# Optimization experiments

Measured on AMD Instinct MI355X. Metric: run time of the kernel, lower is better.

The kernel has to match this reference:

```python
import jax, jax.numpy as jnp
import numpy as np

T, B, C, H, W = 9, 8, 256, 56, 56


def setup_inputs() -> dict:
    key = jax.random.key(0)
    k1, k2, k3, k4 = jax.random.split(key, 4)
    feature_maps_sequence = jax.random.normal(k1, (T, B, C, H, W), dtype=jnp.float32)
    # Conv2d(2C, 1, kernel_size=1): weight [1, 2C, 1, 1], bias [1]
    w = jax.random.normal(k2, (1, 2 * C, 1, 1), dtype=jnp.float32) * 0.02
    b = jax.random.normal(k3, (1,), dtype=jnp.float32) * 0.02
    gamma = jax.random.normal(k4, (1,), dtype=jnp.float32)
    return {"feature_maps_sequence": feature_maps_sequence, "w": w, "b": b, "gamma": gamma}


def reference(feature_maps_sequence, w, b, gamma):
    seq = feature_maps_sequence  # [T, B, C, H, W]
    t = seq.shape[0]
    center = seq[t // 2]  # [B, C, H, W]
    c = seq.shape[2]
    # 1x1 conv over concat([center, frame]) == dot with split weight halves + bias
    w_center = w[0, :c, 0, 0]  # [C]
    w_other = w[0, c:, 0, 0]   # [C]
    score_center = jnp.einsum('bchw,c->bhw', center, w_center)          # [B, H, W]
    score_other = jnp.einsum('tbchw,c->tbhw', seq, w_other)             # [T, B, H, W]
    scores = score_center[None] + score_other + b[0]                    # [T, B, H, W]
    attn = jax.nn.softmax(scores, axis=0)                               # softmax over T
    attended = jnp.einsum('tbhw,tbchw->bchw', attn, seq)                # [B, C, H, W]
    return center + gamma * attended
```

## Files before the change

kernel.cpp:

```cpp
#include <hip/hip_runtime.h>
#include <math.h>

#define TT 9
#define BN 8
#define CC 256
#define HW 3136
#define BHW (BN * HW)
#define PIX 64
#define CHUNKS (HW / PIX)
#define CENTER_T 4

__global__ __launch_bounds__(256) void scores_kernel(
    const float* __restrict__ seq, const float* __restrict__ w,
    float* __restrict__ scores) {
  int blk = blockIdx.x;
  int chunk = blk % CHUNKS;
  int tb = blk / CHUNKS;
  int tid = threadIdx.x;
  int pix = tid & 63;
  int cpart = tid >> 6;

  __shared__ float w_other[CC];
  __shared__ float red[256];
  w_other[tid] = w[CC + tid];
  __syncthreads();

  const float* base = seq + (size_t)tb * CC * HW + chunk * PIX + pix;
  int c0 = cpart * 64;
  float acc = 0.f;
#pragma unroll 8
  for (int cl = 0; cl < 64; ++cl) {
    int c = c0 + cl;
    acc = fmaf(base[(size_t)c * HW], w_other[c], acc);
  }
  red[tid] = acc;
  __syncthreads();
  if (cpart == 0) {
    float s = red[pix] + red[64 + pix] + red[128 + pix] + red[192 + pix];
    scores[(size_t)tb * HW + chunk * PIX + pix] = s;
  }
}

__global__ __launch_bounds__(256) void softmax_kernel(float* __restrict__ scores) {
  int p = blockIdx.x * 256 + threadIdx.x;
  float v[TT];
  float m = -1e30f;
#pragma unroll
  for (int t = 0; t < TT; ++t) {
    v[t] = scores[(size_t)t * BHW + p];
    m = fmaxf(m, v[t]);
  }
  float s = 0.f;
#pragma unroll
  for (int t = 0; t < TT; ++t) {
    v[t] = __expf(v[t] - m);
    s += v[t];
  }
  float inv = 1.f / s;
#pragma unroll
  for (int t = 0; t < TT; ++t) scores[(size_t)t * BHW + p] = v[t] * inv;
}

__global__ __launch_bounds__(256) void attend_kernel(
    const float* __restrict__ seq, const float* __restrict__ attn,
    const float* __restrict__ gamma, float* __restrict__ out) {
  int blk = blockIdx.x;
  int chunk = blk % CHUNKS;
  int rest = blk / CHUNKS;
  int cg = rest % (CC / 16);
  int b = rest / (CC / 16);
  int tid = threadIdx.x;
  int pix = tid & 63;
  int csub = tid >> 6;
  int c0 = cg * 16 + csub * 4;
  int hwp = chunk * PIX + pix;

  float a[TT];
#pragma unroll
  for (int t = 0; t < TT; ++t) a[t] = attn[(size_t)t * BHW + b * HW + hwp];

  float acc[4] = {0.f, 0.f, 0.f, 0.f};
  float cen[4];
#pragma unroll
  for (int t = 0; t < TT; ++t) {
    float at = a[t];
#pragma unroll
    for (int i = 0; i < 4; ++i) {
      float v = seq[(((size_t)t * BN + b) * CC + (c0 + i)) * HW + hwp];
      acc[i] = fmaf(at, v, acc[i]);
      if (t == CENTER_T) cen[i] = v;
    }
  }
  float g = gamma[0];
#pragma unroll
  for (int i = 0; i < 4; ++i)
    out[((size_t)b * CC + (c0 + i)) * HW + hwp] = fmaf(g, acc[i], cen[i]);
}

extern "C" void kernel_launch(void* const* d_in, const int* in_sizes, int n_in,
                              void* d_out, int out_size, void* d_ws, size_t ws_size,
                              hipStream_t stream) {
  const float* seq = (const float*)d_in[0];
  const float* w = (const float*)d_in[1];
  const float* gamma = (const float*)d_in[3];
  float* out = (float*)d_out;
  float* scores = (float*)d_ws;

  scores_kernel<<<TT * BN * CHUNKS, 256, 0, stream>>>(seq, w, scores);
  softmax_kernel<<<BHW / 256, 256, 0, stream>>>(scores);
  attend_kernel<<<BN * (CC / 16) * CHUNKS, 256, 0, stream>>>(seq, scores, gamma, out);
}
```

Measured before the change: 358.4 us.

## Fuse score, softmax and attention into a single per-pixel-chunk kernel

Replaces the three-kernel pipeline (scores, softmax, attend) with one kernel. Each block owns 32 pixels of one batch across all channels and all frames: it computes the frame scores with a shared-memory reduction, applies the softmax in place, then re-reads the same sequence slice to form the weighted sum. This removes the scores round trip through global workspace and two extra launches. The second read of the block's slice may be served from cache because it follows soon after the first. In exchange, each block does 16 channel partitions times 9 frames of strided loads, and coalescing drops to 32-pixel (128-byte) rows.

Result: slower. 541.2 us (+51.0%).

```diff
diff --git a/kernel.cpp b/kernel.cpp
--- a/kernel.cpp
+++ b/kernel.cpp
@@ -5,96 +5,91 @@
 #define BN 8
 #define CC 256
 #define HW 3136
-#define BHW (BN * HW)
-#define PIX 64
+#define PIX 32
 #define CHUNKS (HW / PIX)
+#define CPART 16
+#define CPC (CC / CPART)
 #define CENTER_T 4
 
-__global__ __launch_bounds__(256) void scores_kernel(
+__global__ __launch_bounds__(512) void fused_tfma_kernel(
     const float* __restrict__ seq, const float* __restrict__ w,
-    float* __restrict__ scores) {
-  int blk = blockIdx.x;
-  int chunk = blk % CHUNKS;
-  int tb = blk / CHUNKS;
-  int tid = threadIdx.x;
-  int pix = tid & 63;
-  int cpart = tid >> 6;
-
-  __shared__ float w_other[CC];
-  __shared__ float red[256];
-  w_other[tid] = w[CC + tid];
-  __syncthreads();
-
-  const float* base = seq + (size_t)tb * CC * HW + chunk * PIX + pix;
-  int c0 = cpart * 64;
-  float acc = 0.f;
-#pragma unroll 8
-  for (int cl = 0; cl < 64; ++cl) {
-    int c = c0 + cl;
-    acc = fmaf(base[(size_t)c * HW], w_other[c], acc);
-  }
-  red[tid] = acc;
-  __syncthreads();
-  if (cpart == 0) {
-    float s = red[pix] + red[64 + pix] + red[128 + pix] + red[192 + pix];
-    scores[(size_t)tb * HW + chunk * PIX + pix] = s;
-  }
-}
-
-__global__ __launch_bounds__(256) void softmax_kernel(float* __restrict__ scores) {
-  int p = blockIdx.x * 256 + threadIdx.x;
-  float v[TT];
-  float m = -1e30f;
-#pragma unroll
-  for (int t = 0; t < TT; ++t) {
-    v[t] = scores[(size_t)t * BHW + p];
-    m = fmaxf(m, v[t]);
-  }
-  float s = 0.f;
-#pragma unroll
-  for (int t = 0; t < TT; ++t) {
-    v[t] = __expf(v[t] - m);
-    s += v[t];
-  }
-  float inv = 1.f / s;
-#pragma unroll
-  for (int t = 0; t < TT; ++t) scores[(size_t)t * BHW + p] = v[t] * inv;
-}
-
-__global__ __launch_bounds__(256) void attend_kernel(
-    const float* __restrict__ seq, const float* __restrict__ attn,
     const float* __restrict__ gamma, float* __restrict__ out) {
   int blk = blockIdx.x;
   int chunk = blk % CHUNKS;
-  int rest = blk / CHUNKS;
-  int cg = rest % (CC / 16);
-  int b = rest / (CC / 16);
+  int b = blk / CHUNKS;
+  int hw0 = chunk * PIX;
   int tid = threadIdx.x;
-  int pix = tid & 63;
-  int csub = tid >> 6;
-  int c0 = cg * 16 + csub * 4;
-  int hwp = chunk * PIX + pix;
+  int pix = tid & (PIX - 1);
+  int cpart = tid >> 5;
+  int c0 = cpart * CPC;
 
-  float a[TT];
-#pragma unroll
-  for (int t = 0; t < TT; ++t) a[t] = attn[(size_t)t * BHW + b * HW + hwp];
+  __shared__ float w_o[CC];
+  __shared__ float red[TT * CPART * PIX];
+  __shared__ float sc[TT * PIX];
 
-  float acc[4] = {0.f, 0.f, 0.f, 0.f};
-  float cen[4];
-#pragma unroll
+  if (tid < CC) w_o[tid] = w[CC + tid];
+  __syncthreads();
+
+  const float* base = seq + ((size_t)b * CC) * HW + hw0 + pix;
+
+  #pragma unroll
   for (int t = 0; t < TT; ++t) {
-    float at = a[t];
-#pragma unroll
-    for (int i = 0; i < 4; ++i) {
-      float v = seq[(((size_t)t * BN + b) * CC + (c0 + i)) * HW + hwp];
-      acc[i] = fmaf(at, v, acc[i]);
+    const float* bt = base + (size_t)t * BN * CC * HW;
+    float a = 0.f;
+    #pragma unroll
+    for (int i = 0; i < CPC; ++i)
+      a = fmaf(bt[(size_t)(c0 + i) * HW], w_o[c0 + i], a);
+    red[(t * CPART + cpart) * PIX + pix] = a;
+  }
+  __syncthreads();
+
+  if (tid < TT * PIX) {
+    int t = tid >> 5, p = tid & (PIX - 1);
+    float s = 0.f;
+    #pragma unroll
+    for (int cp = 0; cp < CPART; ++cp) s += red[(t * CPART + cp) * PIX + p];
+    sc[t * PIX + p] = s;
+  }
+  __syncthreads();
+  if (tid < PIX) {
+    float v[TT], m = -1e30f;
+    #pragma unroll
+    for (int t = 0; t < TT; ++t) {
+      v[t] = sc[t * PIX + tid];
+      m = fmaxf(m, v[t]);
+    }
+    float s = 0.f;
+    #pragma unroll
+    for (int t = 0; t < TT; ++t) { v[t] = __expf(v[t] - m); s += v[t]; }
+    float inv = 1.f / s;
+    #pragma unroll
+    for (int t = 0; t < TT; ++t) sc[t * PIX + tid] = v[t] * inv;
+  }
+  __syncthreads();
+
+  float at[TT];
+  #pragma unroll
+  for (int t = 0; t < TT; ++t) at[t] = sc[t * PIX + pix];
+
+  float oacc[CPC], cen[CPC];
+  #pragma unroll
+  for (int i = 0; i < CPC; ++i) oacc[i] = 0.f;
+  #pragma unroll
+  for (int t = 0; t < TT; ++t) {
+    const float* bt = base + (size_t)t * BN * CC * HW;
+    float a = at[t];
+    #pragma unroll
+    for (int i = 0; i < CPC; ++i) {
+      float v = bt[(size_t)(c0 + i) * HW];
+      oacc[i] = fmaf(a, v, oacc[i]);
       if (t == CENTER_T) cen[i] = v;
     }
   }
   float g = gamma[0];
-#pragma unroll
-  for (int i = 0; i < 4; ++i)
-    out[((size_t)b * CC + (c0 + i)) * HW + hwp] = fmaf(g, acc[i], cen[i]);
+  float* ob = out + ((size_t)b * CC) * HW + hw0 + pix;
+  #pragma unroll
+  for (int i = 0; i < CPC; ++i)
+    ob[(size_t)(c0 + i) * HW] = fmaf(g, oacc[i], cen[i]);
 }
 
 extern "C" void kernel_launch(void* const* d_in, const int* in_sizes, int n_in,
@@ -104,9 +99,6 @@
   const float* w = (const float*)d_in[1];
   const float* gamma = (const float*)d_in[3];
   float* out = (float*)d_out;
-  float* scores = (float*)d_ws;
 
-  scores_kernel<<<TT * BN * CHUNKS, 256, 0, stream>>>(seq, w, scores);
-  softmax_kernel<<<BHW / 256, 256, 0, stream>>>(scores);
-  attend_kernel<<<BN * (CC / 16) * CHUNKS, 256, 0, stream>>>(seq, scores, gamma, out);
+  fused_tfma_kernel<<<BN * CHUNKS, 512, 0, stream>>>(seq, w, gamma, out);
 }
```

## Fuse softmax into attend kernel and vectorize loads with float4

Applied to the files above, without the earlier changes.

Removes the separate softmax launch and recomputes the softmax over T inside each attend block from the raw scores. Both the score and attend kernels now use float4 loads and stores over 4 pixels per thread, with 16 pixel-groups by 16 channel slices per block. This cuts one launch and one round trip of the scores buffer, and widens memory transactions. In exchange, each attend block repeats the softmax for its pixels, and each channel group of 64 channels redoes it.

Result: no change. 355.1 us (-0.9%).

```diff
diff --git a/kernel.cpp b/kernel.cpp
--- a/kernel.cpp
+++ b/kernel.cpp
@@ -5,10 +5,11 @@
 #define BN 8
 #define CC 256
 #define HW 3136
+#define HW4 (HW / 4)
 #define BHW (BN * HW)
-#define PIX 64
-#define CHUNKS (HW / PIX)
 #define CENTER_T 4
+#define GPT 16
+#define CHUNKS (HW4 / GPT)
 
 __global__ __launch_bounds__(256) void scores_kernel(
     const float* __restrict__ seq, const float* __restrict__ w,
@@ -17,84 +18,112 @@
   int chunk = blk % CHUNKS;
   int tb = blk / CHUNKS;
   int tid = threadIdx.x;
-  int pix = tid & 63;
-  int cpart = tid >> 6;
+  int g = tid & 15;
+  int cpart = tid >> 4;
+  int c0 = cpart * 16;
+  int px = (chunk * GPT + g) * 4;
 
-  __shared__ float w_other[CC];
-  __shared__ float red[256];
-  w_other[tid] = w[CC + tid];
+  __shared__ float w_o[CC];
+  __shared__ float4 red[16][16];
+  w_o[tid] = w[CC + tid];
   __syncthreads();
 
-  const float* base = seq + (size_t)tb * CC * HW + chunk * PIX + pix;
-  int c0 = cpart * 64;
-  float acc = 0.f;
-#pragma unroll 8
-  for (int cl = 0; cl < 64; ++cl) {
-    int c = c0 + cl;
-    acc = fmaf(base[(size_t)c * HW], w_other[c], acc);
+  const float4* base = (const float4*)(seq + (size_t)tb * CC * HW + px);
+  float4 acc = {0.f, 0.f, 0.f, 0.f};
+  #pragma unroll
+  for (int i = 0; i < 16; ++i) {
+    float4 v = base[(size_t)(c0 + i) * HW4];
+    float wc = w_o[c0 + i];
+    acc.x = fmaf(v.x, wc, acc.x);
+    acc.y = fmaf(v.y, wc, acc.y);
+    acc.z = fmaf(v.z, wc, acc.z);
+    acc.w = fmaf(v.w, wc, acc.w);
   }
-  red[tid] = acc;
+  red[cpart][g] = acc;
   __syncthreads();
-  if (cpart == 0) {
-    float s = red[pix] + red[64 + pix] + red[128 + pix] + red[192 + pix];
-    scores[(size_t)tb * HW + chunk * PIX + pix] = s;
+  if (tid < 16) {
+    float4 s = {0.f, 0.f, 0.f, 0.f};
+    #pragma unroll
+    for (int cp = 0; cp < 16; ++cp) {
+      float4 r = red[cp][tid];
+      s.x += r.x; s.y += r.y; s.z += r.z; s.w += r.w;
+    }
+    *(float4*)(scores + (size_t)tb * HW + (chunk * GPT + tid) * 4) = s;
   }
 }
 
-__global__ __launch_bounds__(256) void softmax_kernel(float* __restrict__ scores) {
-  int p = blockIdx.x * 256 + threadIdx.x;
-  float v[TT];
-  float m = -1e30f;
-#pragma unroll
-  for (int t = 0; t < TT; ++t) {
-    v[t] = scores[(size_t)t * BHW + p];
-    m = fmaxf(m, v[t]);
-  }
-  float s = 0.f;
-#pragma unroll
-  for (int t = 0; t < TT; ++t) {
-    v[t] = __expf(v[t] - m);
-    s += v[t];
-  }
-  float inv = 1.f / s;
-#pragma unroll
-  for (int t = 0; t < TT; ++t) scores[(size_t)t * BHW + p] = v[t] * inv;
-}
-
 __global__ __launch_bounds__(256) void attend_kernel(
-    const float* __restrict__ seq, const float* __restrict__ attn,
+    const float* __restrict__ seq, const float* __restrict__ scores,
     const float* __restrict__ gamma, float* __restrict__ out) {
   int blk = blockIdx.x;
   int chunk = blk % CHUNKS;
   int rest = blk / CHUNKS;
-  int cg = rest % (CC / 16);
-  int b = rest / (CC / 16);
+  int cg = rest & 3;
+  int b = rest >> 2;
   int tid = threadIdx.x;
-  int pix = tid & 63;
-  int csub = tid >> 6;
-  int c0 = cg * 16 + csub * 4;
-  int hwp = chunk * PIX + pix;
+  int g = tid & 15;
+  int csub = tid >> 4;
+  int c0 = cg * 64 + csub * 4;
+  int px = (chunk * GPT + g) * 4;
 
-  float a[TT];
-#pragma unroll
-  for (int t = 0; t < TT; ++t) a[t] = attn[(size_t)t * BHW + b * HW + hwp];
+  float4 att[TT];
+  {
+    const float4* sp = (const float4*)(scores + (size_t)b * HW + px);
+    float4 m = {-1e30f, -1e30f, -1e30f, -1e30f};
+    #pragma unroll
+    for (int t = 0; t < TT; ++t) {
+      att[t] = sp[(size_t)t * (BHW / 4)];
+      m.x = fmaxf(m.x, att[t].x);
+      m.y = fmaxf(m.y, att[t].y);
+      m.z = fmaxf(m.z, att[t].z);
+      m.w = fmaxf(m.w, att[t].w);
+    }
+    float4 s = {0.f, 0.f, 0.f, 0.f};
+    #pragma unroll
+    for (int t = 0; t < TT; ++t) {
+      att[t].x = __expf(att[t].x - m.x); s.x += att[t].x;
+      att[t].y = __expf(att[t].y - m.y); s.y += att[t].y;
+      att[t].z = __expf(att[t].z - m.z); s.z += att[t].z;
+      att[t].w = __expf(att[t].w - m.w); s.w += att[t].w;
+    }
+    float4 inv = {1.f / s.x, 1.f / s.y, 1.f / s.z, 1.f / s.w};
+    #pragma unroll
+    for (int t = 0; t < TT; ++t) {
+      att[t].x *= inv.x; att[t].y *= inv.y;
+      att[t].z *= inv.z; att[t].w *= inv.w;
+    }
+  }
 
-  float acc[4] = {0.f, 0.f, 0.f, 0.f};
-  float cen[4];
-#pragma unroll
+  const float4* base = (const float4*)(seq + ((size_t)b * CC + c0) * HW + px);
+  float4 acc[4];
+  float4 cen[4];
+  #pragma unroll
+  for (int i = 0; i < 4; ++i) acc[i] = {0.f, 0.f, 0.f, 0.f};
+  #pragma unroll
   for (int t = 0; t < TT; ++t) {
-    float at = a[t];
-#pragma unroll
+    const float4* bt = base + (size_t)t * BN * CC * HW4;
+    float4 a = att[t];
+    #pragma unroll
     for (int i = 0; i < 4; ++i) {
-      float v = seq[(((size_t)t * BN + b) * CC + (c0 + i)) * HW + hwp];
-      acc[i] = fmaf(at, v, acc[i]);
+      float4 v = bt[(size_t)i * HW4];
+      acc[i].x = fmaf(a.x, v.x, acc[i].x);
+      acc[i].y = fmaf(a.y, v.y, acc[i].y);
+      acc[i].z = fmaf(a.z, v.z, acc[i].z);
+      acc[i].w = fmaf(a.w, v.w, acc[i].w);
       if (t == CENTER_T) cen[i] = v;
     }
   }
-  float g = gamma[0];
-#pragma unroll
-  for (int i = 0; i < 4; ++i)
-    out[((size_t)b * CC + (c0 + i)) * HW + hwp] = fmaf(g, acc[i], cen[i]);
+  float gm = gamma[0];
+  float4* ob = (float4*)(out + ((size_t)b * CC + c0) * HW + px);
+  #pragma unroll
+  for (int i = 0; i < 4; ++i) {
+    float4 o;
+    o.x = fmaf(gm, acc[i].x, cen[i].x);
+    o.y = fmaf(gm, acc[i].y, cen[i].y);
+    o.z = fmaf(gm, acc[i].z, cen[i].z);
+    o.w = fmaf(gm, acc[i].w, cen[i].w);
+    ob[(size_t)i * HW4] = o;
+  }
 }
 
 extern "C" void kernel_launch(void* const* d_in, const int* in_sizes, int n_in,
@@ -107,6 +136,5 @@
   float* scores = (float*)d_ws;
 
   scores_kernel<<<TT * BN * CHUNKS, 256, 0, stream>>>(seq, w, scores);
-  softmax_kernel<<<BHW / 256, 256, 0, stream>>>(scores);
-  attend_kernel<<<BN * (CC / 16) * CHUNKS, 256, 0, stream>>>(seq, scores, gamma, out);
+  attend_kernel<<<BN * 4 * CHUNKS, 256, 0, stream>>>(seq, scores, gamma, out);
 }
```
